# Optimization experiments

Measured on AMD Instinct MI355X. Metric: run time of the kernel, lower is better.

## Reference

```python
import jax, jax.numpy as jnp
import numpy as np

D_MODEL = 512
MEM_DIM = 64
DECAY_LOGIT_INIT = 2.9444389791664403  # logit(0.95)


def setup_inputs() -> dict:
    key = jax.random.key(0)
    ks = jax.random.split(key, 6)
    B, L = 2, 2048
    x = jax.random.normal(ks[0], (B, L, D_MODEL), dtype=jnp.float32)
    s = 1.0 / np.sqrt(D_MODEL)
    W_q = jax.random.normal(ks[1], (MEM_DIM, D_MODEL), dtype=jnp.float32) * s
    W_k = jax.random.normal(ks[2], (MEM_DIM, D_MODEL), dtype=jnp.float32) * s
    W_v = jax.random.normal(ks[3], (D_MODEL, D_MODEL), dtype=jnp.float32) * s
    W_o = jax.random.normal(ks[4], (D_MODEL, D_MODEL), dtype=jnp.float32) * s
    decay_logit = jnp.asarray(DECAY_LOGIT_INIT, dtype=jnp.float32)
    norm_w = jnp.ones((D_MODEL,), dtype=jnp.float32)
    return {"x": x, "W_q": W_q, "W_k": W_k, "W_v": W_v, "W_o": W_o,
            "decay_logit": decay_logit, "norm_w": norm_w}


def _rms_norm(x, w, eps=1e-6):
    dtype = x.dtype
    x_f = x.astype(jnp.float32)
    rms = jnp.sqrt(jnp.mean(x_f * x_f, axis=-1, keepdims=True) + eps)
    return (x_f / rms).astype(dtype) * w.astype(dtype)


def reference(x, W_q, W_k, W_v, W_o, decay_logit, norm_w):
    B, L, D = x.shape
    M = W_q.shape[0]
    scale = M ** (-0.5)
    phi = lambda t: jax.nn.elu(t) + 1.0  # positive kernel
    queries = phi(x @ W_q.T) * scale          # (B,L,M)
    keys = phi(x @ W_k.T)                     # (B,L,M)
    values = x @ W_v.T                        # (B,L,D)

    decay = jax.nn.sigmoid(decay_logit)
    log_decay = jnp.log(jnp.clip(decay, 1e-6))
    positions = jnp.arange(L, dtype=x.dtype)
    log_cum = jnp.clip(log_decay * positions, -20.0, 20.0)  # (L,)
    exp_neg = jnp.exp(-log_cum)[None, :, None]              # (1,L,1)
    exp_pos = jnp.exp(log_cum)[None, :, None]

    # fast-weight write: M_t = exp_pos_t * cumsum_s<=t exp_neg_s * k_s^T v_s
    kv = keys[..., :, None] * values[..., None, :]          # (B,L,M,D)
    cum_kv = jnp.cumsum(exp_neg[..., None] * kv, axis=1)
    Mem = exp_pos[..., None] * cum_kv                       # (B,L,M,D)

    z = exp_pos * jnp.cumsum(exp_neg * keys, axis=1)        # (B,L,M)

    numerator = jnp.einsum('blm,blmd->bld', queries, Mem)
    denominator = jnp.einsum('blm,blm->bl', queries, z)[..., None] + 1e-6
    out = _rms_norm(numerator / denominator, norm_w)
    return out @ W_o.T
```

## Files before the change

### kernel.cpp

```cpp
#include <hip/hip_runtime.h>
#include <math.h>

#define NB 2
#define LSEQ 2048
#define DM 512
#define MM 64
#define CHK 64
#define NCHUNK 32

typedef __attribute__((ext_vector_type(8))) short short8v;
typedef __attribute__((ext_vector_type(4))) float f32x4;

__device__ __forceinline__ float get_ld(const float* __restrict__ logit) {
    float lg = *logit;
    float dec = 1.0f / (1.0f + expf(-lg));
    dec = fmaxf(dec, 1e-6f);
    return logf(dec);
}
__device__ __forceinline__ float cpos(float ld, int t) {
    return fminf(fmaxf(ld * (float)t, -20.0f), 20.0f);
}
__device__ __forceinline__ float phi_fn(float v) {
    return v > 0.0f ? v + 1.0f : expf(v);
}
__device__ __forceinline__ unsigned short f2bf(float f) {
    unsigned int u = __float_as_uint(f);
    u += 0x7FFFu + ((u >> 16) & 1u);
    return (unsigned short)(u >> 16);
}
__device__ __forceinline__ float bf2f(unsigned short h) {
    unsigned int u = ((unsigned int)h) << 16;
    return __uint_as_float(u);
}
__device__ __forceinline__ uint4 cvt8(const float* __restrict__ p) {
    float4 a = *(const float4*)p;
    float4 b = *(const float4*)(p + 4);
    union { unsigned short u[8]; uint4 v; } r;
    r.u[0] = f2bf(a.x); r.u[1] = f2bf(a.y); r.u[2] = f2bf(a.z); r.u[3] = f2bf(a.w);
    r.u[4] = f2bf(b.x); r.u[5] = f2bf(b.y); r.u[6] = f2bf(b.z); r.u[7] = f2bf(b.w);
    return r.v;
}

__global__ __launch_bounds__(256) void gemm_proj(
    const float* __restrict__ x, const float* __restrict__ W_q,
    const float* __restrict__ W_k, const float* __restrict__ W_v,
    const float* __restrict__ W_o,
    unsigned short* __restrict__ Qh, unsigned short* __restrict__ Kh,
    unsigned short* __restrict__ Vh, unsigned short* __restrict__ Wob)
{
    const int cb = blockIdx.y;
    const int tid = threadIdx.x;
    if (cb == 5) {
        const int stride = 64 * 256;
#pragma unroll
        for (int it = 0; it < 4; ++it) {
            int i = blockIdx.x * 256 + tid + it * stride;
            float4 v = ((const float4*)W_o)[i];
            ushort4 o;
            o.x = f2bf(v.x); o.y = f2bf(v.y); o.z = f2bf(v.z); o.w = f2bf(v.w);
            ((ushort4*)Wob)[i] = o;
        }
        return;
    }

    __shared__ unsigned short As[64][40];
    __shared__ unsigned short Bs[128][40];
    const int brow = blockIdx.x * 64;
    const int lane = tid & 63, wid = tid >> 6;
    const int wr = wid >> 1, wc = wid & 1;
    const int lr = lane & 15, lk = lane >> 4;

    f32x4 acc[2][4];
#pragma unroll
    for (int i = 0; i < 2; ++i)
#pragma unroll
        for (int j = 0; j < 4; ++j) acc[i][j] = (f32x4)(0.f);

    for (int k0 = 0; k0 < DM; k0 += 32) {
        {
            const int r = tid >> 2, kg = tid & 3;
            *(uint4*)&As[r][kg * 8] = cvt8(&x[(size_t)(brow + r) * DM + k0 + kg * 8]);
        }
#pragma unroll
        for (int i = 0; i < 2; ++i) {
            int c = tid * 2 + i;
            int r = c >> 2, kg = c & 3;
            const float* wsrc;
            if (cb == 0)
                wsrc = (r < 64) ? &W_q[(size_t)r * DM + k0 + kg * 8]
                                : &W_k[(size_t)(r - 64) * DM + k0 + kg * 8];
            else
                wsrc = &W_v[(size_t)((cb - 1) * 128 + r) * DM + k0 + kg * 8];
            *(uint4*)&Bs[r][kg * 8] = cvt8(wsrc);
        }
        __syncthreads();
        short8v af[2], bf[4];
#pragma unroll
        for (int mt = 0; mt < 2; ++mt)
            af[mt] = *(const short8v*)&As[wr * 32 + mt * 16 + lr][lk * 8];
#pragma unroll
        for (int nt = 0; nt < 4; ++nt)
            bf[nt] = *(const short8v*)&Bs[wc * 64 + nt * 16 + lr][lk * 8];
#pragma unroll
        for (int mt = 0; mt < 2; ++mt)
#pragma unroll
            for (int nt = 0; nt < 4; ++nt)
                acc[mt][nt] = __builtin_amdgcn_mfma_f32_16x16x32_bf16(
                    af[mt], bf[nt], acc[mt][nt], 0, 0, 0);
        __syncthreads();
    }

#pragma unroll
    for (int mt = 0; mt < 2; ++mt)
#pragma unroll
        for (int nt = 0; nt < 4; ++nt) {
            const int col = wc * 64 + nt * 16 + lr;
#pragma unroll
            for (int j = 0; j < 4; ++j) {
                const int row = brow + wr * 32 + mt * 16 + lk * 4 + j;
                float v = acc[mt][nt][j];
                if (cb == 0) {
                    v = phi_fn(v);
                    if (col < 64)
                        Qh[(size_t)row * MM + col] = f2bf(v * 0.125f);
                    else
                        Kh[(size_t)row * MM + (col - 64)] = f2bf(v);
                } else {
                    Vh[(size_t)row * DM + (cb - 1) * 128 + col] = f2bf(v);
                }
            }
        }
}

__global__ __launch_bounds__(256) void chunk_local_mfma(
    const unsigned short* __restrict__ Qb, const unsigned short* __restrict__ Kb,
    const unsigned short* __restrict__ Vb, const float* __restrict__ logit,
    float* __restrict__ OI, float* __restrict__ DI,
    float* __restrict__ KV, float* __restrict__ KZ)
{
    const int chunk = blockIdx.x, dg = blockIdx.y, b = blockIdx.z;
    const int tid = threadIdx.x;
    const int lane = tid & 63, wid = tid >> 6;
    const int wr = wid >> 1, wc = wid & 1;
    const int lr = lane & 15, lk = lane >> 4;
    const int t0 = chunk * CHK;
    const float ld = get_ld(logit);

    __shared__ unsigned short Qs[64][72];
    __shared__ unsigned short Ks[64][72];
    __shared__ unsigned short As[64][72];
    __shared__ unsigned short Kws[64][66];
    __shared__ unsigned short Vs[64][134];
    __shared__ float wks[64];
    __shared__ float cps[64];
    __shared__ float DIsh[64];

    if (tid < 64) {
        const float c = cpos(ld, t0 + tid);
        cps[tid] = c;
        wks[tid] = expf(cpos(ld, t0 + CHK - 1) - c);
        DIsh[tid] = 0.f;
    }
    __syncthreads();

    const unsigned short* Qg = Qb + ((size_t)b * LSEQ + t0) * MM;
    const unsigned short* Kg = Kb + ((size_t)b * LSEQ + t0) * MM;
#pragma unroll
    for (int l = 0; l < 2; ++l) {
        const int e = tid + l * 256;
        const int r = e >> 3, gq = e & 7;
        *(uint4*)&Qs[r][gq * 8] = *(const uint4*)(Qg + (size_t)e * 8);
        uint4 kraw = *(const uint4*)(Kg + (size_t)e * 8);
        *(uint4*)&Ks[r][gq * 8] = kraw;
        const float w = wks[r];
        const unsigned short* kp = (const unsigned short*)&kraw;
#pragma unroll
        for (int p = 0; p < 4; ++p) {
            ushort2 o;
            o.x = f2bf(w * bf2f(kp[2 * p]));
            o.y = f2bf(w * bf2f(kp[2 * p + 1]));
            *(ushort2*)&Kws[r][gq * 8 + 2 * p] = o;
        }
    }
    const unsigned short* Vg = Vb + ((size_t)b * LSEQ + t0) * DM + dg * 128;
#pragma unroll
    for (int l = 0; l < 4; ++l) {
        const int e = tid + l * 256;
        const int s = e >> 4, gg = e & 15;
        uint4 vr = *(const uint4*)(Vg + (size_t)s * DM + gg * 8);
        const unsigned short* vp = (const unsigned short*)&vr;
#pragma unroll
        for (int p = 0; p < 4; ++p) {
            ushort2 o;
            o.x = vp[2 * p]; o.y = vp[2 * p + 1];
            *(ushort2*)&Vs[s][gg * 8 + 2 * p] = o;
        }
    }
    __syncthreads();

    f32x4 sacc[2][2];
#pragma unroll
    for (int i = 0; i < 2; ++i)
#pragma unroll
        for (int j = 0; j < 2; ++j) sacc[i][j] = (f32x4)(0.f);
#pragma unroll
    for (int ks = 0; ks < 2; ++ks) {
        short8v qa[2], kb2[2];
#pragma unroll
        for (int mt = 0; mt < 2; ++mt)
            qa[mt] = *(const short8v*)&Qs[wr * 32 + mt * 16 + lr][ks * 32 + lk * 8];
#pragma unroll
        for (int nt = 0; nt < 2; ++nt)
            kb2[nt] = *(const short8v*)&Ks[wc * 32 + nt * 16 + lr][ks * 32 + lk * 8];
#pragma unroll
        for (int mt = 0; mt < 2; ++mt)
#pragma unroll
            for (int nt = 0; nt < 2; ++nt)
                sacc[mt][nt] = __builtin_amdgcn_mfma_f32_16x16x32_bf16(
                    qa[mt], kb2[nt], sacc[mt][nt], 0, 0, 0);
    }

#pragma unroll
    for (int mt = 0; mt < 2; ++mt) {
#pragma unroll
        for (int j = 0; j < 4; ++j) {
            const int t = wr * 32 + mt * 16 + lk * 4 + j;
            const float ct = cps[t];
            float rowpart = 0.f;
#pragma unroll
            for (int nt = 0; nt < 2; ++nt) {
                const int s = wc * 32 + nt * 16 + lr;
                float v = sacc[mt][nt][j];
                v = (s <= t) ? v * expf(ct - cps[s]) : 0.f;
                rowpart += v;
                As[t][s] = f2bf(v);
            }
            rowpart += __shfl_xor(rowpart, 1);
            rowpart += __shfl_xor(rowpart, 2);
            rowpart += __shfl_xor(rowpart, 4);
            rowpart += __shfl_xor(rowpart, 8);
            if (lr == 0) atomicAdd(&DIsh[t], rowpart);
        }
    }
    __syncthreads();

    if (dg == 0) {
        if (tid < 64) DI[(size_t)b * LSEQ + t0 + tid] = DIsh[tid];
        if (tid >= 64 && tid < 128) {
            const int m = tid - 64;
            float z = 0.f;
#pragma unroll
            for (int s = 0; s < 64; ++s) z += wks[s] * bf2f(Ks[s][m]);
            KZ[((size_t)b * NCHUNK + chunk) * MM + m] = z;
        }
    }

    f32x4 aO[2][4], aK[2][4];
#pragma unroll
    for (int i = 0; i < 2; ++i)
#pragma unroll
        for (int j = 0; j < 4; ++j) { aO[i][j] = (f32x4)(0.f); aK[i][j] = (f32x4)(0.f); }

#pragma unroll
    for (int ks = 0; ks < 2; ++ks) {
        short8v vf[4];
#pragma unroll
        for (int nt = 0; nt < 4; ++nt) {
            unsigned short* vp = (unsigned short*)&vf[nt];
            const int n = wc * 64 + nt * 16 + lr;
#pragma unroll
            for (int e = 0; e < 8; ++e)
                vp[e] = Vs[ks * 32 + lk * 8 + e][n];
        }
        short8v af2[2], kf2[2];
#pragma unroll
        for (int mt = 0; mt < 2; ++mt) {
            const int row = wr * 32 + mt * 16 + lr;
            af2[mt] = *(const short8v*)&As[row][ks * 32 + lk * 8];
            unsigned short* kp = (unsigned short*)&kf2[mt];
#pragma unroll
            for (int e = 0; e < 8; ++e)
                kp[e] = Kws[ks * 32 + lk * 8 + e][row];
        }
#pragma unroll
        for (int mt = 0; mt < 2; ++mt)
#pragma unroll
            for (int nt = 0; nt < 4; ++nt) {
                aO[mt][nt] = __builtin_amdgcn_mfma_f32_16x16x32_bf16(
                    af2[mt], vf[nt], aO[mt][nt], 0, 0, 0);
                aK[mt][nt] = __builtin_amdgcn_mfma_f32_16x16x32_bf16(
                    kf2[mt], vf[nt], aK[mt][nt], 0, 0, 0);
            }
    }

    float* OIb = OI + ((size_t)b * LSEQ + t0) * DM + dg * 128;
    float* KVb = KV + ((size_t)b * NCHUNK + chunk) * MM * DM + dg * 128;
#pragma unroll
    for (int mt = 0; mt < 2; ++mt)
#pragma unroll
        for (int nt = 0; nt < 4; ++nt) {
            const int col = wc * 64 + nt * 16 + lr;
#pragma unroll
            for (int j = 0; j < 4; ++j) {
                const int row = wr * 32 + mt * 16 + lk * 4 + j;
                OIb[(size_t)row * DM + col] = aO[mt][nt][j];
                KVb[(size_t)row * DM + col] = aK[mt][nt][j];
            }
        }
}

__global__ __launch_bounds__(256) void state_scan(
    const float* __restrict__ KV, const float* __restrict__ KZ,
    const float* __restrict__ logit,
    unsigned short* __restrict__ SS, float* __restrict__ ZS)
{
    const int g = blockIdx.x * 256 + threadIdx.x;
    const int b = g >> 15;
    const int rem = g & 32767;
    const int m = rem >> 9;
    const int d = rem & 511;
    const float ld = get_ld(logit);
    const size_t base = (((size_t)b * NCHUNK) * MM + m) * DM + d;
    const size_t cstride = (size_t)MM * DM;

    float v[NCHUNK];
#pragma unroll
    for (int i = 0; i < NCHUNK; ++i) v[i] = KV[base + (size_t)i * cstride];

    float s = 0.f, cprev = 0.f;
#pragma unroll
    for (int i = 0; i < NCHUNK; ++i) {
        const float ce = cpos(ld, i * CHK + CHK - 1);
        const float lam = expf(ce - cprev);
        cprev = ce;
        SS[base + (size_t)i * cstride] = f2bf(s);
        s = lam * s + v[i];
    }
    if (d == 0) {
        float zs = 0.f;
        cprev = 0.f;
#pragma unroll
        for (int i = 0; i < NCHUNK; ++i) {
            const float ce = cpos(ld, i * CHK + CHK - 1);
            const float lam = expf(ce - cprev);
            cprev = ce;
            const int zi = (b * NCHUNK + i) * MM + m;
            ZS[zi] = zs;
            zs = lam * zs + KZ[zi];
        }
    }
}

__global__ __launch_bounds__(256) void combine_rms(
    const unsigned short* __restrict__ Qb, const unsigned short* __restrict__ SSb,
    const float* __restrict__ ZS, const float* __restrict__ OI,
    const float* __restrict__ DI, const float* __restrict__ logit,
    const float* __restrict__ norm_w, unsigned short* __restrict__ NRM)
{
    const int chunk = blockIdx.x, half = blockIdx.y, b = blockIdx.z;
    const int tid = threadIdx.x;
    const int lane = tid & 63, w = tid >> 6;
    const int lr = lane & 15, lk = lane >> 4;
    const int t0 = chunk * CHK;
    const int r0 = half * 32;
    const float ld = get_ld(logit);

    __shared__ unsigned short Qs[32][72];
    __shared__ unsigned short Ssh[64][514];
    __shared__ float wsh[512];
    __shared__ float gv[32], invden[32], xsq[32], rinv[32];

    {
        const unsigned short* Qg = Qb + ((size_t)b * LSEQ + t0 + r0) * MM;
        const int r = tid >> 3, g8 = tid & 7;
        *(uint4*)&Qs[r][g8 * 8] = *(const uint4*)(Qg + (size_t)tid * 8);
    }
    {
        const unsigned short* Sg = SSb + ((size_t)(b * NCHUNK + chunk) * MM) * DM;
#pragma unroll
        for (int l = 0; l < 16; ++l) {
            const int e = tid + l * 256;
            const int m = e >> 6, g8 = e & 63;
            uint4 v = *(const uint4*)(Sg + (size_t)m * DM + g8 * 8);
            const unsigned short* vp = (const unsigned short*)&v;
#pragma unroll
            for (int p = 0; p < 4; ++p) {
                ushort2 o; o.x = vp[2 * p]; o.y = vp[2 * p + 1];
                *(ushort2*)&Ssh[m][g8 * 8 + 2 * p] = o;
            }
        }
    }
    wsh[tid] = norm_w[tid];
    wsh[tid + 256] = norm_w[tid + 256];
    if (tid < 32) {
        const float cprev = (chunk > 0) ? cpos(ld, t0 - 1) : 0.f;
        gv[tid] = expf(cpos(ld, t0 + r0 + tid) - cprev);
        xsq[tid] = 0.f;
    }
    __syncthreads();

    if (tid < 32) {
        const float* zp = ZS + ((size_t)b * NCHUNK + chunk) * MM;
        float a = 0.f;
#pragma unroll
        for (int m = 0; m < MM; ++m) a += bf2f(Qs[tid][m]) * zp[m];
        invden[tid] = 1.0f /
            (gv[tid] * a + DI[(size_t)b * LSEQ + t0 + r0 + tid] + 1e-6f);
    }

    f32x4 acc[2][8];
#pragma unroll
    for (int i = 0; i < 2; ++i)
#pragma unroll
        for (int j = 0; j < 8; ++j) acc[i][j] = (f32x4)(0.f);

#pragma unroll
    for (int ks = 0; ks < 2; ++ks) {
        short8v vf[8];
#pragma unroll
        for (int nt = 0; nt < 8; ++nt) {
            unsigned short* vp = (unsigned short*)&vf[nt];
            const int col = w * 128 + nt * 16 + lr;
#pragma unroll
            for (int e = 0; e < 8; ++e)
                vp[e] = Ssh[ks * 32 + lk * 8 + e][col];
        }
        short8v af[2];
#pragma unroll
        for (int mt = 0; mt < 2; ++mt)
            af[mt] = *(const short8v*)&Qs[mt * 16 + lr][ks * 32 + lk * 8];
#pragma unroll
        for (int mt = 0; mt < 2; ++mt)
#pragma unroll
            for (int nt = 0; nt < 8; ++nt)
                acc[mt][nt] = __builtin_amdgcn_mfma_f32_16x16x32_bf16(
                    af[mt], vf[nt], acc[mt][nt], 0, 0, 0);
    }
    __syncthreads();

    const float* OIb = OI + ((size_t)b * LSEQ + t0 + r0) * DM;
#pragma unroll
    for (int mt = 0; mt < 2; ++mt) {
#pragma unroll
        for (int j = 0; j < 4; ++j) {
            const int row = mt * 16 + lk * 4 + j;
            const float g = gv[row];
            const float inv = invden[row];
            float part = 0.f;
#pragma unroll
            for (int nt = 0; nt < 8; ++nt) {
                const int col = w * 128 + nt * 16 + lr;
                float v = g * acc[mt][nt][j] + OIb[(size_t)row * DM + col];
                float xx = v * inv;
                acc[mt][nt][j] = xx;
                part += xx * xx;
            }
            part += __shfl_xor(part, 1);
            part += __shfl_xor(part, 2);
            part += __shfl_xor(part, 4);
            part += __shfl_xor(part, 8);
            if (lr == 0) atomicAdd(&xsq[row], part);
        }
    }
    __syncthreads();
    if (tid < 32)
        rinv[tid] = 1.0f / sqrtf(xsq[tid] * (1.0f / (float)DM) + 1e-6f);
    __syncthreads();

    unsigned short* NRMc = NRM + ((size_t)b * LSEQ + t0 + r0) * DM;
#pragma unroll
    for (int mt = 0; mt < 2; ++mt)
#pragma unroll
        for (int j = 0; j < 4; ++j) {
            const int row = mt * 16 + lk * 4 + j;
            const float r = rinv[row];
#pragma unroll
            for (int nt = 0; nt < 8; ++nt) {
                const int col = w * 128 + nt * 16 + lr;
                NRMc[(size_t)row * DM + col] = f2bf(acc[mt][nt][j] * r * wsh[col]);
            }
        }
}

__global__ __launch_bounds__(256) void gemm_out(
    const unsigned short* __restrict__ Xb, const unsigned short* __restrict__ Wb,
    float* __restrict__ C)
{
    __shared__ unsigned short As[64][40];
    __shared__ unsigned short Bs[128][40];
    const int brow = blockIdx.x * 64;
    const int bcol = blockIdx.y * 128;
    const int tid = threadIdx.x;
    const int lane = tid & 63, wid = tid >> 6;
    const int wr = wid >> 1, wc = wid & 1;
    const int lr = lane & 15, lk = lane >> 4;

    f32x4 acc[2][4];
#pragma unroll
    for (int i = 0; i < 2; ++i)
#pragma unroll
        for (int j = 0; j < 4; ++j) acc[i][j] = (f32x4)(0.f);

    for (int k0 = 0; k0 < DM; k0 += 32) {
        {
            const int r = tid >> 2, kg = tid & 3;
            *(uint4*)&As[r][kg * 8] =
                *(const uint4*)&Xb[(size_t)(brow + r) * DM + k0 + kg * 8];
        }
#pragma unroll
        for (int i = 0; i < 2; ++i) {
            int c = tid * 2 + i;
            int r = c >> 2, kg = c & 3;
            *(uint4*)&Bs[r][kg * 8] =
                *(const uint4*)&Wb[(size_t)(bcol + r) * DM + k0 + kg * 8];
        }
        __syncthreads();
        short8v af[2], bf[4];
#pragma unroll
        for (int mt = 0; mt < 2; ++mt)
            af[mt] = *(const short8v*)&As[wr * 32 + mt * 16 + lr][lk * 8];
#pragma unroll
        for (int nt = 0; nt < 4; ++nt)
            bf[nt] = *(const short8v*)&Bs[wc * 64 + nt * 16 + lr][lk * 8];
#pragma unroll
        for (int mt = 0; mt < 2; ++mt)
#pragma unroll
            for (int nt = 0; nt < 4; ++nt)
                acc[mt][nt] = __builtin_amdgcn_mfma_f32_16x16x32_bf16(
                    af[mt], bf[nt], acc[mt][nt], 0, 0, 0);
        __syncthreads();
    }

#pragma unroll
    for (int mt = 0; mt < 2; ++mt)
#pragma unroll
        for (int nt = 0; nt < 4; ++nt) {
            const int row0 = brow + wr * 32 + mt * 16 + lk * 4;
            const int col = bcol + wc * 64 + nt * 16 + lr;
#pragma unroll
            for (int j = 0; j < 4; ++j)
                C[(size_t)(row0 + j) * DM + col] = acc[mt][nt][j];
        }
}

extern "C" void kernel_launch(void* const* d_in, const int* in_sizes, int n_in,
                              void* d_out, int out_size, void* d_ws, size_t ws_size,
                              hipStream_t stream) {
    const float* x      = (const float*)d_in[0];
    const float* W_q    = (const float*)d_in[1];
    const float* W_k    = (const float*)d_in[2];
    const float* W_v    = (const float*)d_in[3];
    const float* W_o    = (const float*)d_in[4];
    const float* logit  = (const float*)d_in[5];
    const float* norm_w = (const float*)d_in[6];
    float* out = (float*)d_out;

    const size_t BLM = (size_t)NB * LSEQ * MM;
    const size_t BLD = (size_t)NB * LSEQ * DM;
    const size_t BL  = (size_t)NB * LSEQ;
    const size_t BNCMD = (size_t)NB * NCHUNK * MM * DM;
    const size_t BNCM  = (size_t)NB * NCHUNK * MM;
    const size_t WSZ = (size_t)DM * DM;

    float* ws = (float*)d_ws;
    float* OIp  = ws;
    float* DIp  = OIp + BLD;
    float* KVp  = DIp + BL;
    float* KZp  = KVp + BNCMD;
    float* ZSp  = KZp + BNCM;
    unsigned short* Wob16 = (unsigned short*)(ZSp + BNCM);
    unsigned short* Qb16 = Wob16 + WSZ;
    unsigned short* Kb16 = Qb16 + BLM;
    unsigned short* Vb16 = Kb16 + BLM;
    unsigned short* SSb  = Vb16 + BLD;
    unsigned short* NRMb = SSb + BNCMD;

    gemm_proj<<<dim3(64, 6), 256, 0, stream>>>(x, W_q, W_k, W_v, W_o,
                                               Qb16, Kb16, Vb16, Wob16);
    chunk_local_mfma<<<dim3(NCHUNK, 4, NB), 256, 0, stream>>>(
        Qb16, Kb16, Vb16, logit, OIp, DIp, KVp, KZp);
    state_scan<<<dim3(256), 256, 0, stream>>>(KVp, KZp, logit, SSb, ZSp);
    combine_rms<<<dim3(NCHUNK, 2, NB), 256, 0, stream>>>(
        Qb16, SSb, ZSp, OIp, DIp, logit, norm_w, NRMb);
    gemm_out<<<dim3(64, 4), 256, 0, stream>>>(NRMb, Wob16, out);
}
```

Before: 64.36 us.

## Fuse output projection into combine kernel and store intermediates in bf16

```diff
diff --git a/kernel.cpp b/kernel.cpp
--- a/kernel.cpp
+++ b/kernel.cpp
@@ -135,8 +135,8 @@
 __global__ __launch_bounds__(256) void chunk_local_mfma(
     const unsigned short* __restrict__ Qb, const unsigned short* __restrict__ Kb,
     const unsigned short* __restrict__ Vb, const float* __restrict__ logit,
-    float* __restrict__ OI, float* __restrict__ DI,
-    float* __restrict__ KV, float* __restrict__ KZ)
+    unsigned short* __restrict__ OI, float* __restrict__ DI,
+    unsigned short* __restrict__ KV, float* __restrict__ KZ)
 {
     const int chunk = blockIdx.x, dg = blockIdx.y, b = blockIdx.z;
     const int tid = threadIdx.x;
@@ -293,8 +293,8 @@
             }
     }
 
-    float* OIb = OI + ((size_t)b * LSEQ + t0) * DM + dg * 128;
-    float* KVb = KV + ((size_t)b * NCHUNK + chunk) * MM * DM + dg * 128;
+    unsigned short* OIb = OI + ((size_t)b * LSEQ + t0) * DM + dg * 128;
+    unsigned short* KVb = KV + ((size_t)b * NCHUNK + chunk) * MM * DM + dg * 128;
 #pragma unroll
     for (int mt = 0; mt < 2; ++mt)
 #pragma unroll
@@ -303,14 +303,14 @@
 #pragma unroll
             for (int j = 0; j < 4; ++j) {
                 const int row = wr * 32 + mt * 16 + lk * 4 + j;
-                OIb[(size_t)row * DM + col] = aO[mt][nt][j];
-                KVb[(size_t)row * DM + col] = aK[mt][nt][j];
+                OIb[(size_t)row * DM + col] = f2bf(aO[mt][nt][j]);
+                KVb[(size_t)row * DM + col] = f2bf(aK[mt][nt][j]);
             }
         }
 }
 
 __global__ __launch_bounds__(256) void state_scan(
-    const float* __restrict__ KV, const float* __restrict__ KZ,
+    const unsigned short* __restrict__ KV, const float* __restrict__ KZ,
     const float* __restrict__ logit,
     unsigned short* __restrict__ SS, float* __restrict__ ZS)
 {
@@ -325,7 +325,7 @@
 
     float v[NCHUNK];
 #pragma unroll
-    for (int i = 0; i < NCHUNK; ++i) v[i] = KV[base + (size_t)i * cstride];
+    for (int i = 0; i < NCHUNK; ++i) v[i] = bf2f(KV[base + (size_t)i * cstride]);
 
     float s = 0.f, cprev = 0.f;
 #pragma unroll
@@ -351,11 +351,12 @@
     }
 }
 
-__global__ __launch_bounds__(256) void combine_rms(
+__global__ __launch_bounds__(256) void combine_out(
     const unsigned short* __restrict__ Qb, const unsigned short* __restrict__ SSb,
-    const float* __restrict__ ZS, const float* __restrict__ OI,
+    const float* __restrict__ ZS, const unsigned short* __restrict__ OI,
     const float* __restrict__ DI, const float* __restrict__ logit,
-    const float* __restrict__ norm_w, unsigned short* __restrict__ NRM)
+    const float* __restrict__ norm_w, const unsigned short* __restrict__ Wob,
+    float* __restrict__ out)
 {
     const int chunk = blockIdx.x, half = blockIdx.y, b = blockIdx.z;
     const int tid = threadIdx.x;
@@ -366,7 +367,10 @@
     const float ld = get_ld(logit);
 
     __shared__ unsigned short Qs[32][72];
-    __shared__ unsigned short Ssh[64][514];
+    __shared__ union {
+        unsigned short Ssh[64][514];
+        unsigned short Nsh[32][520];
+    } U;
     __shared__ float wsh[512];
     __shared__ float gv[32], invden[32], xsq[32], rinv[32];
 
@@ -386,7 +390,7 @@
 #pragma unroll
             for (int p = 0; p < 4; ++p) {
                 ushort2 o; o.x = vp[2 * p]; o.y = vp[2 * p + 1];
-                *(ushort2*)&Ssh[m][g8 * 8 + 2 * p] = o;
+                *(ushort2*)&U.Ssh[m][g8 * 8 + 2 * p] = o;
             }
         }
     }
@@ -423,7 +427,7 @@
             const int col = w * 128 + nt * 16 + lr;
 #pragma unroll
             for (int e = 0; e < 8; ++e)
-                vp[e] = Ssh[ks * 32 + lk * 8 + e][col];
+                vp[e] = U.Ssh[ks * 32 + lk * 8 + e][col];
         }
         short8v af[2];
 #pragma unroll
@@ -438,7 +442,7 @@
     }
     __syncthreads();
 
-    const float* OIb = OI + ((size_t)b * LSEQ + t0 + r0) * DM;
+    const unsigned short* OIb = OI + ((size_t)b * LSEQ + t0 + r0) * DM;
 #pragma unroll
     for (int mt = 0; mt < 2; ++mt) {
 #pragma unroll
@@ -450,7 +454,7 @@
 #pragma unroll
             for (int nt = 0; nt < 8; ++nt) {
                 const int col = w * 128 + nt * 16 + lr;
-                float v = g * acc[mt][nt][j] + OIb[(size_t)row * DM + col];
+                float v = g * acc[mt][nt][j] + bf2f(OIb[(size_t)row * DM + col]);
                 float xx = v * inv;
                 acc[mt][nt][j] = xx;
                 part += xx * xx;
@@ -467,7 +471,6 @@
         rinv[tid] = 1.0f / sqrtf(xsq[tid] * (1.0f / (float)DM) + 1e-6f);
     __syncthreads();
 
-    unsigned short* NRMc = NRM + ((size_t)b * LSEQ + t0 + r0) * DM;
 #pragma unroll
     for (int mt = 0; mt < 2; ++mt)
 #pragma unroll
@@ -477,69 +480,45 @@
 #pragma unroll
             for (int nt = 0; nt < 8; ++nt) {
                 const int col = w * 128 + nt * 16 + lr;
-                NRMc[(size_t)row * DM + col] = f2bf(acc[mt][nt][j] * r * wsh[col]);
-            }
-        }
-}
-
-__global__ __launch_bounds__(256) void gemm_out(
-    const unsigned short* __restrict__ Xb, const unsigned short* __restrict__ Wb,
-    float* __restrict__ C)
-{
-    __shared__ unsigned short As[64][40];
-    __shared__ unsigned short Bs[128][40];
-    const int brow = blockIdx.x * 64;
-    const int bcol = blockIdx.y * 128;
-    const int tid = threadIdx.x;
-    const int lane = tid & 63, wid = tid >> 6;
-    const int wr = wid >> 1, wc = wid & 1;
-    const int lr = lane & 15, lk = lane >> 4;
-
-    f32x4 acc[2][4];
+                U.Nsh[row][col] = f2bf(acc[mt][nt][j] * r * wsh[col]);
+            }
+        }
+    __syncthreads();
+
+    f32x4 acc2[2][8];
 #pragma unroll
     for (int i = 0; i < 2; ++i)
 #pragma unroll
-        for (int j = 0; j < 4; ++j) acc[i][j] = (f32x4)(0.f);
-
+        for (int j = 0; j < 8; ++j) acc2[i][j] = (f32x4)(0.f);
+
+    const unsigned short* Wow = Wob + (size_t)(w * 128) * DM;
+#pragma unroll 2
     for (int k0 = 0; k0 < DM; k0 += 32) {
-        {
-            const int r = tid >> 2, kg = tid & 3;
-            *(uint4*)&As[r][kg * 8] =
-                *(const uint4*)&Xb[(size_t)(brow + r) * DM + k0 + kg * 8];
-        }
-#pragma unroll
-        for (int i = 0; i < 2; ++i) {
-            int c = tid * 2 + i;
-            int r = c >> 2, kg = c & 3;
-            *(uint4*)&Bs[r][kg * 8] =
-                *(const uint4*)&Wb[(size_t)(bcol + r) * DM + k0 + kg * 8];
-        }
-        __syncthreads();
-        short8v af[2], bf[4];
-#pragma unroll
-        for (int mt = 0; mt < 2; ++mt)
-            af[mt] = *(const short8v*)&As[wr * 32 + mt * 16 + lr][lk * 8];
-#pragma unroll
-        for (int nt = 0; nt < 4; ++nt)
-            bf[nt] = *(const short8v*)&Bs[wc * 64 + nt * 16 + lr][lk * 8];
-#pragma unroll
-        for (int mt = 0; mt < 2; ++mt)
-#pragma unroll
-            for (int nt = 0; nt < 4; ++nt)
-                acc[mt][nt] = __builtin_amdgcn_mfma_f32_16x16x32_bf16(
-                    af[mt], bf[nt], acc[mt][nt], 0, 0, 0);
-        __syncthreads();
-    }
-
+        short8v af[2];
+#pragma unroll
+        for (int mt = 0; mt < 2; ++mt)
+            af[mt] = *(const short8v*)&U.Nsh[mt * 16 + lr][k0 + lk * 8];
+#pragma unroll
+        for (int nt = 0; nt < 8; ++nt) {
+            short8v bfr = *(const short8v*)&Wow[(size_t)(nt * 16 + lr) * DM + k0 + lk * 8];
+            acc2[0][nt] = __builtin_amdgcn_mfma_f32_16x16x32_bf16(
+                af[0], bfr, acc2[0][nt], 0, 0, 0);
+            acc2[1][nt] = __builtin_amdgcn_mfma_f32_16x16x32_bf16(
+                af[1], bfr, acc2[1][nt], 0, 0, 0);
+        }
+    }
+
+    float* outb = out + ((size_t)b * LSEQ + t0 + r0) * DM;
 #pragma unroll
     for (int mt = 0; mt < 2; ++mt)
 #pragma unroll
-        for (int nt = 0; nt < 4; ++nt) {
-            const int row0 = brow + wr * 32 + mt * 16 + lk * 4;
-            const int col = bcol + wc * 64 + nt * 16 + lr;
-#pragma unroll
-            for (int j = 0; j < 4; ++j)
-                C[(size_t)(row0 + j) * DM + col] = acc[mt][nt][j];
+        for (int nt = 0; nt < 8; ++nt) {
+            const int col = w * 128 + nt * 16 + lr;
+#pragma unroll
+            for (int j = 0; j < 4; ++j) {
+                const int row = mt * 16 + lk * 4 + j;
+                outb[(size_t)row * DM + col] = acc2[mt][nt][j];
+            }
         }
 }
 
@@ -563,24 +542,22 @@
     const size_t WSZ = (size_t)DM * DM;
 
     float* ws = (float*)d_ws;
-    float* OIp  = ws;
-    float* DIp  = OIp + BLD;
-    float* KVp  = DIp + BL;
-    float* KZp  = KVp + BNCMD;
-    float* ZSp  = KZp + BNCM;
-    unsigned short* Wob16 = (unsigned short*)(ZSp + BNCM);
+    float* DIp = ws;
+    float* KZp = DIp + BL;
+    float* ZSp = KZp + BNCM;
+    unsigned short* OIb  = (unsigned short*)(ZSp + BNCM);
+    unsigned short* KVb  = OIb + BLD;
+    unsigned short* SSb  = KVb + BNCMD;
+    unsigned short* Wob16 = SSb + BNCMD;
     unsigned short* Qb16 = Wob16 + WSZ;
     unsigned short* Kb16 = Qb16 + BLM;
     unsigned short* Vb16 = Kb16 + BLM;
-    unsigned short* SSb  = Vb16 + BLD;
-    unsigned short* NRMb = SSb + BNCMD;
 
     gemm_proj<<<dim3(64, 6), 256, 0, stream>>>(x, W_q, W_k, W_v, W_o,
                                                Qb16, Kb16, Vb16, Wob16);
     chunk_local_mfma<<<dim3(NCHUNK, 4, NB), 256, 0, stream>>>(
-        Qb16, Kb16, Vb16, logit, OIp, DIp, KVp, KZp);
-    state_scan<<<dim3(256), 256, 0, stream>>>(KVp, KZp, logit, SSb, ZSp);
-    combine_rms<<<dim3(NCHUNK, 2, NB), 256, 0, stream>>>(
-        Qb16, SSb, ZSp, OIp, DIp, logit, norm_w, NRMb);
-    gemm_out<<<dim3(64, 4), 256, 0, stream>>>(NRMb, Wob16, out);
-}
+        Qb16, Kb16, Vb16, logit, OIb, DIp, KVb, KZp);
+    state_scan<<<dim3(256), 256, 0, stream>>>(KVb, KZp, logit, SSb, ZSp);
+    combine_out<<<dim3(NCHUNK, 2, NB), 256, 0, stream>>>(
+        Qb16, SSb, ZSp, OIb, DIp, logit, norm_w, Wob16, out);
+}
```

New measurement: 68.51 us. 1.06x slower.
